# Performance work log

Hardware: AMD Instinct MI355X
Metric: run time of the kernel (lower is better)

## Reference

```python
import jax, jax.numpy as jnp
import numpy as np

NUM_HEADS = 16

def setup_inputs() -> dict:
    B, S, H = 2, 2048, 1024
    Hh = H // 2
    key = jax.random.key(0)
    ks = jax.random.split(key, 16)
    sd = 1.0 / np.sqrt(H)
    sdh = 1.0 / np.sqrt(Hh)
    return {
        "query": jax.random.normal(ks[0], (B, S, H), jnp.float32),
        "key_in": jax.random.normal(ks[1], (B, S, H), jnp.float32),
        "value": jax.random.normal(ks[2], (B, S, H), jnp.float32),
        "direction_signal": jax.random.randint(ks[3], (B, S), 0, 3, jnp.int64),
        # Linear weights stored as (in, out); y = x @ W + b (same math as torch x @ W.T + b)
        "Wq_w": jax.random.normal(ks[4], (H, H), jnp.float32) * sd,
        "Wq_b": jnp.zeros((H,), jnp.float32),
        "Wk_w": jax.random.normal(ks[5], (H, H), jnp.float32) * sd,
        "Wk_b": jnp.zeros((H,), jnp.float32),
        "Wv_w": jax.random.normal(ks[6], (H, H), jnp.float32) * sd,
        "Wv_b": jnp.zeros((H,), jnp.float32),
        "ds1_w": jax.random.normal(ks[7], (H, Hh), jnp.float32) * sd,
        "ds1_b": jnp.zeros((Hh,), jnp.float32),
        "ds2_w": jax.random.normal(ks[8], (Hh, NUM_HEADS), jnp.float32) * sdh,
        "ds2_b": jnp.zeros((NUM_HEADS,), jnp.float32),
        "fo_w": jax.random.normal(ks[9], (H, H), jnp.float32) * sd,
        "fo_b": jnp.zeros((H,), jnp.float32),
    }

def reference(query, key_in, value, direction_signal,
              Wq_w, Wq_b, Wk_w, Wk_b, Wv_w, Wv_b,
              ds1_w, ds1_b, ds2_w, ds2_b, fo_w, fo_b):
    B, S, H = query.shape
    nh = NUM_HEADS
    hd = H // nh
    scale = np.sqrt(hd).astype(np.float32)

    def split_heads(x):  # (B,S,H) -> (B,nh,S,hd)
        return x.reshape(B, S, nh, hd).transpose(0, 2, 1, 3)

    Q = split_heads(query @ Wq_w + Wq_b)
    K = split_heads(key_in @ Wk_w + Wk_b)
    V = split_heads(value @ Wv_w + Wv_b)

    scores = jnp.einsum('bhqd,bhkd->bhqk', Q, K) / scale

    # direction bias: per-(batch, head, query) additive scalar broadcast over keys
    # torch nn.GELU default is exact (erf) -> approximate=False
    dir_w = jax.nn.gelu(query @ ds1_w + ds1_b, approximate=False) @ ds2_w + ds2_b  # (B,S,nh)
    scores = scores + 0.3 * dir_w.transpose(0, 2, 1)[..., None]

    attention = jax.nn.softmax(scores, axis=-1)
    # dropout is identity in eval/reference mode
    context = jnp.einsum('bhqk,bhkd->bqhd', attention, V).reshape(B, S, H)
    output = context @ fo_w + fo_b
    return output, attention
```

## Files before the change

### kernel.cpp

```cpp
#include <hip/hip_runtime.h>


typedef unsigned short u16;
typedef unsigned int   u32;
typedef _Float16       f16;
typedef f16   half8   __attribute__((ext_vector_type(8)));
typedef float floatx4 __attribute__((ext_vector_type(4)));
typedef u32   u32x4   __attribute__((ext_vector_type(4)));

union V8 { u16 u[8]; u32x4 v; };

__device__ __forceinline__ u16 f16_bits(float f){
    union { f16 h; u16 u; } x; x.h = (f16)f; return x.u;
}

template<typename TI>
__global__ __launch_bounds__(256) void transpose_k(
    const TI* __restrict__ in, u16* __restrict__ out,
    long irs, long ors, int zdiv, long ibs0, long ibs1, long obs0, long obs1)
{
    __shared__ u16 tile[64][72];
    int z = blockIdx.z;
    const TI* ip = in  + (long)(z / zdiv) * ibs0 + (long)(z % zdiv) * ibs1;
    u16*      op = out + (long)(z / zdiv) * obs0 + (long)(z % zdiv) * obs1;
    long r0 = (long)blockIdx.y * 64, c0 = (long)blockIdx.x * 64;
    int t = threadIdx.x;
    int r = t >> 2, cs = (t & 3) * 16;
#pragma unroll
    for (int j = 0; j < 16; j++){
        TI v = ip[(r0 + r) * irs + c0 + cs + j];
        if (sizeof(TI) == 4) tile[r][cs + j] = f16_bits((float)v);
        else                 tile[r][cs + j] = (u16)v;
    }
    __syncthreads();
#pragma unroll
    for (int j = 0; j < 16; j++){
        op[(c0 + r) * ors + r0 + cs + j] = tile[cs + j][r];
    }
}

__global__ __launch_bounds__(256) void transpose_w4(
    const float* __restrict__ w0, const float* __restrict__ w1,
    const float* __restrict__ w2, const float* __restrict__ w3,
    u16* __restrict__ o0, u16* __restrict__ o1,
    u16* __restrict__ o2, u16* __restrict__ o3)
{
    __shared__ u16 tile[64][72];
    int z = blockIdx.z;
    const float* ip = (z == 0) ? w0 : (z == 1) ? w1 : (z == 2) ? w2 : w3;
    u16*         op = (z == 0) ? o0 : (z == 1) ? o1 : (z == 2) ? o2 : o3;
    long r0 = (long)blockIdx.y * 64, c0 = (long)blockIdx.x * 64;
    int t = threadIdx.x;
    int r = t >> 2, cs = (t & 3) * 16;
#pragma unroll
    for (int j = 0; j < 16; j++)
        tile[r][cs + j] = f16_bits(ip[(r0 + r) * 1024 + c0 + cs + j]);
    __syncthreads();
#pragma unroll
    for (int j = 0; j < 16; j++)
        op[(c0 + r) * 1024 + r0 + cs + j] = tile[cs + j][r];
}

template<bool A_F32, bool OUT_F32>
__global__ __launch_bounds__(256) void gemm_bt(
    const void* __restrict__ Av, const u16* __restrict__ BT,
    const float* __restrict__ bias, void* __restrict__ Cv,
    int M, int N, int K, float out_scale)
{
    __shared__ u16 Alds[64][40];
    __shared__ u16 Blds[64][40];
    int m0 = blockIdx.y * 64, n0 = blockIdx.x * 64;
    int t = threadIdx.x, w = t >> 6, lane = t & 63, quad = lane >> 4, l16 = lane & 15;
    int wm = (w >> 1) * 32, wn = (w & 1) * 32;
    const floatx4 zero4 = {0.f, 0.f, 0.f, 0.f};
    floatx4 acc[2][2];
#pragma unroll
    for (int i = 0; i < 2; i++)
#pragma unroll
        for (int j = 0; j < 2; j++) acc[i][j] = zero4;

    int srow = t >> 2, scol = (t & 3) * 8;
    const float* Apf = (const float*)Av + (long)(m0 + srow) * K + scol;
    const u16*   Aph = (const u16*)Av   + (long)(m0 + srow) * K + scol;
    const u16*   Bp  = BT + (long)(n0 + srow) * K + scol;

    for (int k0 = 0; k0 < K; k0 += 32){
        __syncthreads();
        V8 va, vb;
        if (A_F32){
            floatx4 a0 = *(const floatx4*)(Apf + k0);
            floatx4 a1 = *(const floatx4*)(Apf + k0 + 4);
#pragma unroll
            for (int j = 0; j < 4; j++){
                va.u[j]     = f16_bits(a0[j]);
                va.u[4 + j] = f16_bits(a1[j]);
            }
        } else {
            va.v = *(const u32x4*)(Aph + k0);
        }
        vb.v = *(const u32x4*)(Bp + k0);
        *(u32x4*)&Alds[srow][scol] = va.v;
        *(u32x4*)&Blds[srow][scol] = vb.v;
        __syncthreads();
        half8 a0 = *(const half8*)&Alds[wm + l16][quad * 8];
        half8 a1 = *(const half8*)&Alds[wm + 16 + l16][quad * 8];
        half8 b0 = *(const half8*)&Blds[wn + l16][quad * 8];
        half8 b1 = *(const half8*)&Blds[wn + 16 + l16][quad * 8];
        acc[0][0] = __builtin_amdgcn_mfma_f32_16x16x32_f16(a0, b0, acc[0][0], 0, 0, 0);
        acc[0][1] = __builtin_amdgcn_mfma_f32_16x16x32_f16(a0, b1, acc[0][1], 0, 0, 0);
        acc[1][0] = __builtin_amdgcn_mfma_f32_16x16x32_f16(a1, b0, acc[1][0], 0, 0, 0);
        acc[1][1] = __builtin_amdgcn_mfma_f32_16x16x32_f16(a1, b1, acc[1][1], 0, 0, 0);
    }

#pragma unroll
    for (int mi = 0; mi < 2; mi++)
#pragma unroll
        for (int ni = 0; ni < 2; ni++){
            int n = n0 + wn + ni * 16 + l16;
            float bv = bias[n];
#pragma unroll
            for (int r = 0; r < 4; r++){
                int m = m0 + wm + mi * 16 + quad * 4 + r;
                float v = (acc[mi][ni][r] + bv) * out_scale;
                if (OUT_F32) ((float*)Cv)[(long)m * N + n] = v;
                else         ((u16*)Cv)[(long)m * N + n]   = f16_bits(v);
            }
        }
}

__global__ __launch_bounds__(256) void gemm_qkv(
    const float* __restrict__ Aq, const float* __restrict__ Ak, const float* __restrict__ Avv,
    const u16* __restrict__ Bq, const u16* __restrict__ Bk, const u16* __restrict__ Bv,
    const float* __restrict__ bq, const float* __restrict__ bk, const float* __restrict__ bv,
    u16* __restrict__ Cq, u16* __restrict__ Ck, u16* __restrict__ Cv,
    int M, int N, int K)
{
    __shared__ u16 Alds[64][40];
    __shared__ u16 Blds[64][40];
    int z = blockIdx.z;
    const float* A    = (z == 0) ? Aq : (z == 1) ? Ak : Avv;
    const u16*   BT   = (z == 0) ? Bq : (z == 1) ? Bk : Bv;
    const float* bias = (z == 0) ? bq : (z == 1) ? bk : bv;
    u16*         C    = (z == 0) ? Cq : (z == 1) ? Ck : Cv;
    float out_scale   = (z == 0) ? 0.125f : 1.0f;

    int m0 = blockIdx.y * 64, n0 = blockIdx.x * 64;
    int t = threadIdx.x, w = t >> 6, lane = t & 63, quad = lane >> 4, l16 = lane & 15;
    int wm = (w >> 1) * 32, wn = (w & 1) * 32;
    const floatx4 zero4 = {0.f, 0.f, 0.f, 0.f};
    floatx4 acc[2][2];
#pragma unroll
    for (int i = 0; i < 2; i++)
#pragma unroll
        for (int j = 0; j < 2; j++) acc[i][j] = zero4;

    int srow = t >> 2, scol = (t & 3) * 8;
    const float* Apf = A + (long)(m0 + srow) * K + scol;
    const u16*   Bp  = BT + (long)(n0 + srow) * K + scol;

    for (int k0 = 0; k0 < K; k0 += 32){
        __syncthreads();
        V8 va, vb;
        floatx4 a0 = *(const floatx4*)(Apf + k0);
        floatx4 a1 = *(const floatx4*)(Apf + k0 + 4);
#pragma unroll
        for (int j = 0; j < 4; j++){
            va.u[j]     = f16_bits(a0[j]);
            va.u[4 + j] = f16_bits(a1[j]);
        }
        vb.v = *(const u32x4*)(Bp + k0);
        *(u32x4*)&Alds[srow][scol] = va.v;
        *(u32x4*)&Blds[srow][scol] = vb.v;
        __syncthreads();
        half8 af0 = *(const half8*)&Alds[wm + l16][quad * 8];
        half8 af1 = *(const half8*)&Alds[wm + 16 + l16][quad * 8];
        half8 bf0 = *(const half8*)&Blds[wn + l16][quad * 8];
        half8 bf1 = *(const half8*)&Blds[wn + 16 + l16][quad * 8];
        acc[0][0] = __builtin_amdgcn_mfma_f32_16x16x32_f16(af0, bf0, acc[0][0], 0, 0, 0);
        acc[0][1] = __builtin_amdgcn_mfma_f32_16x16x32_f16(af0, bf1, acc[0][1], 0, 0, 0);
        acc[1][0] = __builtin_amdgcn_mfma_f32_16x16x32_f16(af1, bf0, acc[1][0], 0, 0, 0);
        acc[1][1] = __builtin_amdgcn_mfma_f32_16x16x32_f16(af1, bf1, acc[1][1], 0, 0, 0);
    }

#pragma unroll
    for (int mi = 0; mi < 2; mi++)
#pragma unroll
        for (int ni = 0; ni < 2; ni++){
            int n = n0 + wn + ni * 16 + l16;
            float bv = bias[n];
#pragma unroll
            for (int r = 0; r < 4; r++){
                int m = m0 + wm + mi * 16 + quad * 4 + r;
                C[(long)m * N + n] = f16_bits((acc[mi][ni][r] + bv) * out_scale);
            }
        }
}

#define S_LEN 2048
#define NH 16
#define HD 64

__global__ __launch_bounds__(256) void attn_k(
    const u16* __restrict__ Q, const u16* __restrict__ K,
    const u16* __restrict__ VT, float* __restrict__ attn,
    u16* __restrict__ ctx)
{
    __shared__ u16 Klds[64][72];
    __shared__ u16 Vlds[64][72];
    __shared__ u16 P0  [64][72];
    __shared__ u16 P1  [64][72];

    int bx0 = blockIdx.x;
    int bx = ((bx0 & 7) << 6) | (bx0 >> 3);
    int qb = bx & 15, h = (bx >> 4) & 15, b = bx >> 8;
    int qbase = qb * 128;
    int t = threadIdx.x, w = t >> 6, lane = t & 63, quad = lane >> 4, l16 = lane & 15;
    const u16* Qp  = Q + (long)b * S_LEN * 1024 + h * HD;
    const u16* Kp  = K + (long)b * S_LEN * 1024 + h * HD;
    const u16* VTp = VT + ((long)(b * NH + h)) * HD * S_LEN;

    const u16* q0p = Qp + (long)(qbase + w * 16 + l16) * 1024;
    const u16* q1p = q0p + 64 * 1024;
    half8 qa0 = *(const half8*)(q0p + quad * 8);
    half8 qa1 = *(const half8*)(q0p + 32 + quad * 8);
    half8 qb0 = *(const half8*)(q1p + quad * 8);
    half8 qb1 = *(const half8*)(q1p + 32 + quad * 8);

    const floatx4 zero4 = {0.f, 0.f, 0.f, 0.f};
    int srow = t >> 2, sseg = (t & 3) * 16;

    const u16* kptr = Kp + (long)srow * 1024 + sseg;
    const u16* vptr = VTp + (long)srow * S_LEN + sseg;

    float lsum0 = 0.f, lsum1 = 0.f;
    {
        u32x4 pk0 = *(const u32x4*)(kptr);
        u32x4 pk1 = *(const u32x4*)(kptr + 8);
        const u16* kp = kptr + 64 * 1024;
        for (int it = 0; it < 32; ++it){
            __syncthreads();
            *(u32x4*)&Klds[srow][sseg]     = pk0;
            *(u32x4*)&Klds[srow][sseg + 8] = pk1;
            __syncthreads();
            if (it < 31){
                pk0 = *(const u32x4*)(kp);
                pk1 = *(const u32x4*)(kp + 8);
                kp += 64 * 1024;
            }
#pragma unroll
            for (int kt = 0; kt < 4; kt++){
                half8 kf0 = *(const half8*)&Klds[kt * 16 + l16][quad * 8];
                half8 kf1 = *(const half8*)&Klds[kt * 16 + l16][32 + quad * 8];
                floatx4 s0 = __builtin_amdgcn_mfma_f32_16x16x32_f16(kf0, qa0, zero4, 0, 0, 0);
                s0 = __builtin_amdgcn_mfma_f32_16x16x32_f16(kf1, qa1, s0, 0, 0, 0);
                floatx4 s1 = __builtin_amdgcn_mfma_f32_16x16x32_f16(kf0, qb0, zero4, 0, 0, 0);
                s1 = __builtin_amdgcn_mfma_f32_16x16x32_f16(kf1, qb1, s1, 0, 0, 0);
#pragma unroll
                for (int r = 0; r < 4; r++){
                    lsum0 += __expf(s0[r]);
                    lsum1 += __expf(s1[r]);
                }
            }
        }
    }
    lsum0 += __shfl_xor(lsum0, 16); lsum0 += __shfl_xor(lsum0, 32);
    lsum1 += __shfl_xor(lsum1, 16); lsum1 += __shfl_xor(lsum1, 32);
    float linv0 = 1.f / lsum0, linv1 = 1.f / lsum1;

    floatx4 cta[4], ctb[4];
#pragma unroll
    for (int dt = 0; dt < 4; dt++){ cta[dt] = zero4; ctb[dt] = zero4; }

    long aq0 = ((long)(b * NH + h) * S_LEN + qbase + w * 16 + l16) * S_LEN;
    long aq1 = aq0 + 64L * S_LEN;

    {
        u32x4 pk0 = *(const u32x4*)(kptr);
        u32x4 pk1 = *(const u32x4*)(kptr + 8);
        u32x4 pv0 = *(const u32x4*)(vptr);
        u32x4 pv1 = *(const u32x4*)(vptr + 8);
        const u16* kp = kptr + 64 * 1024;
        const u16* vp = vptr + 64;
        for (int it = 0; it < 32; ++it){
            int k0 = it * 64;
            __syncthreads();
            *(u32x4*)&Klds[srow][sseg]     = pk0;
            *(u32x4*)&Klds[srow][sseg + 8] = pk1;
            *(u32x4*)&Vlds[srow][sseg]     = pv0;
            *(u32x4*)&Vlds[srow][sseg + 8] = pv1;
            __syncthreads();
            if (it < 31){
                pk0 = *(const u32x4*)(kp);
                pk1 = *(const u32x4*)(kp + 8);
                pv0 = *(const u32x4*)(vp);
                pv1 = *(const u32x4*)(vp + 8);
                kp += 64 * 1024;
                vp += 64;
            }
#pragma unroll
            for (int kt = 0; kt < 4; kt++){
                half8 kf0 = *(const half8*)&Klds[kt * 16 + l16][quad * 8];
                half8 kf1 = *(const half8*)&Klds[kt * 16 + l16][32 + quad * 8];
                floatx4 s0 = __builtin_amdgcn_mfma_f32_16x16x32_f16(kf0, qa0, zero4, 0, 0, 0);
                s0 = __builtin_amdgcn_mfma_f32_16x16x32_f16(kf1, qa1, s0, 0, 0, 0);
                floatx4 s1 = __builtin_amdgcn_mfma_f32_16x16x32_f16(kf0, qb0, zero4, 0, 0, 0);
                s1 = __builtin_amdgcn_mfma_f32_16x16x32_f16(kf1, qb1, s1, 0, 0, 0);
                floatx4 p0;
#pragma unroll
                for (int r = 0; r < 4; r++) p0[r] = __expf(s0[r]) * linv0;
                __builtin_nontemporal_store(p0,
                    (floatx4*)(attn + aq0 + k0 + kt * 16 + quad * 4));
                u32 pa01 = (u32)f16_bits(p0[0]) | ((u32)f16_bits(p0[1]) << 16);
                u32 pa23 = (u32)f16_bits(p0[2]) | ((u32)f16_bits(p0[3]) << 16);
                *(u32*)&P0[w * 16 + l16][kt * 16 + quad * 4]     = pa01;
                *(u32*)&P0[w * 16 + l16][kt * 16 + quad * 4 + 2] = pa23;
                floatx4 p1;
#pragma unroll
                for (int r = 0; r < 4; r++) p1[r] = __expf(s1[r]) * linv1;
                __builtin_nontemporal_store(p1,
                    (floatx4*)(attn + aq1 + k0 + kt * 16 + quad * 4));
                u32 pb01 = (u32)f16_bits(p1[0]) | ((u32)f16_bits(p1[1]) << 16);
                u32 pb23 = (u32)f16_bits(p1[2]) | ((u32)f16_bits(p1[3]) << 16);
                *(u32*)&P1[w * 16 + l16][kt * 16 + quad * 4]     = pb01;
                *(u32*)&P1[w * 16 + l16][kt * 16 + quad * 4 + 2] = pb23;
            }
#pragma unroll
            for (int kk = 0; kk < 2; kk++){
                half8 pf0 = *(const half8*)&P0[w * 16 + l16][kk * 32 + quad * 8];
                half8 pf1 = *(const half8*)&P1[w * 16 + l16][kk * 32 + quad * 8];
#pragma unroll
                for (int dt = 0; dt < 4; dt++){
                    half8 vf = *(const half8*)&Vlds[dt * 16 + l16][kk * 32 + quad * 8];
                    cta[dt] = __builtin_amdgcn_mfma_f32_16x16x32_f16(vf, pf0, cta[dt], 0, 0, 0);
                    ctb[dt] = __builtin_amdgcn_mfma_f32_16x16x32_f16(vf, pf1, ctb[dt], 0, 0, 0);
                }
            }
        }
    }

#pragma unroll
    for (int dt = 0; dt < 4; dt++)
#pragma unroll
        for (int r = 0; r < 4; r++){
            P0[w * 16 + l16][dt * 16 + quad * 4 + r] = f16_bits(cta[dt][r]);
            P1[w * 16 + l16][dt * 16 + quad * 4 + r] = f16_bits(ctb[dt][r]);
        }
    __syncthreads();
    {
        V8 o0, o1, o2, o3;
#pragma unroll
        for (int j = 0; j < 8; j++){
            o0.u[j] = P0[srow][sseg + j];
            o1.u[j] = P0[srow][sseg + 8 + j];
            o2.u[j] = P1[srow][sseg + j];
            o3.u[j] = P1[srow][sseg + 8 + j];
        }
        long c0 = ((long)b * S_LEN + qbase + srow) * 1024 + h * HD + sseg;
        long c1 = c0 + 64L * 1024;
        *(u32x4*)(ctx + c0)     = o0.v;
        *(u32x4*)(ctx + c0 + 8) = o1.v;
        *(u32x4*)(ctx + c1)     = o2.v;
        *(u32x4*)(ctx + c1 + 8) = o3.v;
    }
}

extern "C" void kernel_launch(void* const* d_in, const int* in_sizes, int n_in,
                              void* d_out, int out_size, void* d_ws, size_t ws_size,
                              hipStream_t stream)
{
    (void)in_sizes; (void)n_in; (void)out_size; (void)ws_size;
    const float* query  = (const float*)d_in[0];
    const float* key_in = (const float*)d_in[1];
    const float* value  = (const float*)d_in[2];
    const float* Wq_w = (const float*)d_in[4];  const float* Wq_b = (const float*)d_in[5];
    const float* Wk_w = (const float*)d_in[6];  const float* Wk_b = (const float*)d_in[7];
    const float* Wv_w = (const float*)d_in[8];  const float* Wv_b = (const float*)d_in[9];
    const float* fo_w = (const float*)d_in[14]; const float* fo_b = (const float*)d_in[15];

    float* out  = (float*)d_out;
    float* attn = out + 4194304L;

    u16* ws  = (u16*)d_ws;
    u16* WqT = ws;
    u16* WkT = WqT + 1048576;
    u16* WvT = WkT + 1048576;
    u16* foT = WvT + 1048576;
    u16* Qm  = foT + 1048576;
    u16* Km  = Qm  + 4194304;
    u16* Vm  = Km  + 4194304;
    u16* VTm = Vm  + 4194304;
    u16* CTX = VTm + 4194304;

    dim3 blk(256);
    transpose_w4<<<dim3(16,16,4), blk, 0, stream>>>(
        Wq_w, Wk_w, Wv_w, fo_w, WqT, WkT, WvT, foT);
    gemm_qkv<<<dim3(16,64,3), blk, 0, stream>>>(
        query, key_in, value, WqT, WkT, WvT, Wq_b, Wk_b, Wv_b,
        Qm, Km, Vm, 4096, 1024, 1024);
    transpose_k<u16><<<dim3(1,32,32), blk, 0, stream>>>(Vm, VTm, 1024, 2048, 16,
        2048L*1024, 64, 16L*64*2048, 64L*2048);
    attn_k<<<dim3(512), blk, 0, stream>>>(Qm, Km, VTm, attn, CTX);
    gemm_bt<false,true><<<dim3(16,64), blk, 0, stream>>>(CTX, foT, fo_b, out, 4096,1024,1024, 1.0f);
}
```

Measured before the change: 818.5 us.

## Use 128x128 GEMM tiles with direct global-to-LDS loads and exp2 softmax

The QKV and output projection GEMMs move from 64x64 to 128x128 block tiles with 4x4 MFMA accumulators per wave, and half-precision operands are loaded straight into LDS with global_load_lds. The attention kernel switches from __expf to the hardware exp2, with log2(e) folded into the Q projection scale, and packs probabilities to fp16 with cvt_pkrtz. The aim is more data reuse per LDS load, fewer conversion instructions, and cheaper exponentials. In exchange, LDS is unpadded (possible bank conflicts), there is more register pressure, and the GEMM grids are smaller.

After: 794.9 us. -2.9%, faster.

```diff
diff --git a/kernel.cpp b/kernel.cpp
--- a/kernel.cpp
+++ b/kernel.cpp
@@ -5,14 +5,21 @@
 typedef unsigned int   u32;
 typedef _Float16       f16;
 typedef f16   half8   __attribute__((ext_vector_type(8)));
+typedef f16   h2f16   __attribute__((ext_vector_type(2)));
 typedef float floatx4 __attribute__((ext_vector_type(4)));
 typedef u32   u32x4   __attribute__((ext_vector_type(4)));
+typedef u32   u32x2   __attribute__((ext_vector_type(2)));
 
 union V8 { u16 u[8]; u32x4 v; };
 
 __device__ __forceinline__ u16 f16_bits(float f){
     union { f16 h; u16 u; } x; x.h = (f16)f; return x.u;
 }
+
+#define GLDS16(gsrc, ldst) \
+    __builtin_amdgcn_global_load_lds( \
+        (const __attribute__((address_space(1))) void*)(gsrc), \
+        (__attribute__((address_space(3))) void*)(ldst), 16, 0, 0)
 
 template<typename TI>
 __global__ __launch_bounds__(256) void transpose_k(
@@ -62,138 +69,116 @@
 }
 
 template<bool A_F32, bool OUT_F32>
-__global__ __launch_bounds__(256) void gemm_bt(
+__device__ __forceinline__ void gemm128_body(
     const void* __restrict__ Av, const u16* __restrict__ BT,
     const float* __restrict__ bias, void* __restrict__ Cv,
-    int M, int N, int K, float out_scale)
-{
-    __shared__ u16 Alds[64][40];
-    __shared__ u16 Blds[64][40];
-    int m0 = blockIdx.y * 64, n0 = blockIdx.x * 64;
+    int M, int N, int K, float out_scale,
+    u16* Ald, u16* Bld, int m0, int n0)
+{
     int t = threadIdx.x, w = t >> 6, lane = t & 63, quad = lane >> 4, l16 = lane & 15;
-    int wm = (w >> 1) * 32, wn = (w & 1) * 32;
+    int wm = (w >> 1) * 64, wn = (w & 1) * 64;
     const floatx4 zero4 = {0.f, 0.f, 0.f, 0.f};
-    floatx4 acc[2][2];
-#pragma unroll
-    for (int i = 0; i < 2; i++)
-#pragma unroll
-        for (int j = 0; j < 2; j++) acc[i][j] = zero4;
-
-    int srow = t >> 2, scol = (t & 3) * 8;
-    const float* Apf = (const float*)Av + (long)(m0 + srow) * K + scol;
-    const u16*   Aph = (const u16*)Av   + (long)(m0 + srow) * K + scol;
-    const u16*   Bp  = BT + (long)(n0 + srow) * K + scol;
+    floatx4 acc[4][4];
+#pragma unroll
+    for (int i = 0; i < 4; i++)
+#pragma unroll
+        for (int j = 0; j < 4; j++) acc[i][j] = zero4;
+
+    int grow = w * 16 + (lane >> 2);
+    int gcol = (lane & 3) * 8;
+    const u16* Bsrc0 = BT + (long)(n0 + grow) * K + gcol;
+    const u16* Bsrc1 = BT + (long)(n0 + 64 + grow) * K + gcol;
+    u16* Bdst0 = Bld + w * 512;
+    u16* Bdst1 = Bld + 2048 + w * 512;
+
+    int arow = t >> 1, acol = (t & 1) * 16;
+    const float* Afp = (const float*)Av + (long)(m0 + arow) * K + acol;
+    u16* Adst = Ald + arow * 32 + acol;
+    const u16* Asrc0 = (const u16*)Av + (long)(m0 + grow) * K + gcol;
+    const u16* Asrc1 = (const u16*)Av + (long)(m0 + 64 + grow) * K + gcol;
+    u16* Adst0 = Ald + w * 512;
+    u16* Adst1 = Ald + 2048 + w * 512;
 
     for (int k0 = 0; k0 < K; k0 += 32){
         __syncthreads();
-        V8 va, vb;
+        GLDS16(Bsrc0 + k0, Bdst0);
+        GLDS16(Bsrc1 + k0, Bdst1);
         if (A_F32){
-            floatx4 a0 = *(const floatx4*)(Apf + k0);
-            floatx4 a1 = *(const floatx4*)(Apf + k0 + 4);
+            floatx4 a0 = *(const floatx4*)(Afp + k0);
+            floatx4 a1 = *(const floatx4*)(Afp + k0 + 4);
+            floatx4 a2 = *(const floatx4*)(Afp + k0 + 8);
+            floatx4 a3 = *(const floatx4*)(Afp + k0 + 12);
+            V8 x, y;
 #pragma unroll
             for (int j = 0; j < 4; j++){
-                va.u[j]     = f16_bits(a0[j]);
-                va.u[4 + j] = f16_bits(a1[j]);
-            }
+                x.u[j] = f16_bits(a0[j]); x.u[4 + j] = f16_bits(a1[j]);
+                y.u[j] = f16_bits(a2[j]); y.u[4 + j] = f16_bits(a3[j]);
+            }
+            *(u32x4*)Adst       = x.v;
+            *(u32x4*)(Adst + 8) = y.v;
         } else {
-            va.v = *(const u32x4*)(Aph + k0);
-        }
-        vb.v = *(const u32x4*)(Bp + k0);
-        *(u32x4*)&Alds[srow][scol] = va.v;
-        *(u32x4*)&Blds[srow][scol] = vb.v;
+            GLDS16(Asrc0 + k0, Adst0);
+            GLDS16(Asrc1 + k0, Adst1);
+        }
         __syncthreads();
-        half8 a0 = *(const half8*)&Alds[wm + l16][quad * 8];
-        half8 a1 = *(const half8*)&Alds[wm + 16 + l16][quad * 8];
-        half8 b0 = *(const half8*)&Blds[wn + l16][quad * 8];
-        half8 b1 = *(const half8*)&Blds[wn + 16 + l16][quad * 8];
-        acc[0][0] = __builtin_amdgcn_mfma_f32_16x16x32_f16(a0, b0, acc[0][0], 0, 0, 0);
-        acc[0][1] = __builtin_amdgcn_mfma_f32_16x16x32_f16(a0, b1, acc[0][1], 0, 0, 0);
-        acc[1][0] = __builtin_amdgcn_mfma_f32_16x16x32_f16(a1, b0, acc[1][0], 0, 0, 0);
-        acc[1][1] = __builtin_amdgcn_mfma_f32_16x16x32_f16(a1, b1, acc[1][1], 0, 0, 0);
-    }
-
-#pragma unroll
-    for (int mi = 0; mi < 2; mi++)
-#pragma unroll
-        for (int ni = 0; ni < 2; ni++){
-            int n = n0 + wn + ni * 16 + l16;
+        half8 af[4], bf[4];
+#pragma unroll
+        for (int i = 0; i < 4; i++)
+            af[i] = *(const half8*)&Ald[(wm + i * 16 + l16) * 32 + quad * 8];
+#pragma unroll
+        for (int j = 0; j < 4; j++)
+            bf[j] = *(const half8*)&Bld[(wn + j * 16 + l16) * 32 + quad * 8];
+#pragma unroll
+        for (int i = 0; i < 4; i++)
+#pragma unroll
+            for (int j = 0; j < 4; j++)
+                acc[i][j] = __builtin_amdgcn_mfma_f32_16x16x32_f16(af[i], bf[j], acc[i][j], 0, 0, 0);
+    }
+
+#pragma unroll
+    for (int i = 0; i < 4; i++)
+#pragma unroll
+        for (int j = 0; j < 4; j++){
+            int n = n0 + wn + j * 16 + l16;
             float bv = bias[n];
 #pragma unroll
             for (int r = 0; r < 4; r++){
-                int m = m0 + wm + mi * 16 + quad * 4 + r;
-                float v = (acc[mi][ni][r] + bv) * out_scale;
+                int m = m0 + wm + i * 16 + quad * 4 + r;
+                float v = (acc[i][j][r] + bv) * out_scale;
                 if (OUT_F32) ((float*)Cv)[(long)m * N + n] = v;
                 else         ((u16*)Cv)[(long)m * N + n]   = f16_bits(v);
             }
         }
 }
 
-__global__ __launch_bounds__(256) void gemm_qkv(
+__global__ __launch_bounds__(256) void gemm128_qkv(
     const float* __restrict__ Aq, const float* __restrict__ Ak, const float* __restrict__ Avv,
     const u16* __restrict__ Bq, const u16* __restrict__ Bk, const u16* __restrict__ Bv,
     const float* __restrict__ bq, const float* __restrict__ bk, const float* __restrict__ bv,
     u16* __restrict__ Cq, u16* __restrict__ Ck, u16* __restrict__ Cv,
     int M, int N, int K)
 {
-    __shared__ u16 Alds[64][40];
-    __shared__ u16 Blds[64][40];
+    __shared__ u16 Ald[4096];
+    __shared__ u16 Bld[4096];
     int z = blockIdx.z;
     const float* A    = (z == 0) ? Aq : (z == 1) ? Ak : Avv;
     const u16*   BT   = (z == 0) ? Bq : (z == 1) ? Bk : Bv;
     const float* bias = (z == 0) ? bq : (z == 1) ? bk : bv;
     u16*         C    = (z == 0) ? Cq : (z == 1) ? Ck : Cv;
-    float out_scale   = (z == 0) ? 0.125f : 1.0f;
-
-    int m0 = blockIdx.y * 64, n0 = blockIdx.x * 64;
-    int t = threadIdx.x, w = t >> 6, lane = t & 63, quad = lane >> 4, l16 = lane & 15;
-    int wm = (w >> 1) * 32, wn = (w & 1) * 32;
-    const floatx4 zero4 = {0.f, 0.f, 0.f, 0.f};
-    floatx4 acc[2][2];
-#pragma unroll
-    for (int i = 0; i < 2; i++)
-#pragma unroll
-        for (int j = 0; j < 2; j++) acc[i][j] = zero4;
-
-    int srow = t >> 2, scol = (t & 3) * 8;
-    const float* Apf = A + (long)(m0 + srow) * K + scol;
-    const u16*   Bp  = BT + (long)(n0 + srow) * K + scol;
-
-    for (int k0 = 0; k0 < K; k0 += 32){
-        __syncthreads();
-        V8 va, vb;
-        floatx4 a0 = *(const floatx4*)(Apf + k0);
-        floatx4 a1 = *(const floatx4*)(Apf + k0 + 4);
-#pragma unroll
-        for (int j = 0; j < 4; j++){
-            va.u[j]     = f16_bits(a0[j]);
-            va.u[4 + j] = f16_bits(a1[j]);
-        }
-        vb.v = *(const u32x4*)(Bp + k0);
-        *(u32x4*)&Alds[srow][scol] = va.v;
-        *(u32x4*)&Blds[srow][scol] = vb.v;
-        __syncthreads();
-        half8 af0 = *(const half8*)&Alds[wm + l16][quad * 8];
-        half8 af1 = *(const half8*)&Alds[wm + 16 + l16][quad * 8];
-        half8 bf0 = *(const half8*)&Blds[wn + l16][quad * 8];
-        half8 bf1 = *(const half8*)&Blds[wn + 16 + l16][quad * 8];
-        acc[0][0] = __builtin_amdgcn_mfma_f32_16x16x32_f16(af0, bf0, acc[0][0], 0, 0, 0);
-        acc[0][1] = __builtin_amdgcn_mfma_f32_16x16x32_f16(af0, bf1, acc[0][1], 0, 0, 0);
-        acc[1][0] = __builtin_amdgcn_mfma_f32_16x16x32_f16(af1, bf0, acc[1][0], 0, 0, 0);
-        acc[1][1] = __builtin_amdgcn_mfma_f32_16x16x32_f16(af1, bf1, acc[1][1], 0, 0, 0);
-    }
-
-#pragma unroll
-    for (int mi = 0; mi < 2; mi++)
-#pragma unroll
-        for (int ni = 0; ni < 2; ni++){
-            int n = n0 + wn + ni * 16 + l16;
-            float bv = bias[n];
-#pragma unroll
-            for (int r = 0; r < 4; r++){
-                int m = m0 + wm + mi * 16 + quad * 4 + r;
-                C[(long)m * N + n] = f16_bits((acc[mi][ni][r] + bv) * out_scale);
-            }
-        }
+    float scale       = (z == 0) ? 0.125f * 1.4426950408889634f : 1.0f;
+    gemm128_body<true, false>(A, BT, bias, C, M, N, K, scale,
+                              Ald, Bld, blockIdx.y * 128, blockIdx.x * 128);
+}
+
+__global__ __launch_bounds__(256) void gemm128_ctx(
+    const u16* __restrict__ A, const u16* __restrict__ BT,
+    const float* __restrict__ bias, float* __restrict__ C,
+    int M, int N, int K)
+{
+    __shared__ u16 Ald[4096];
+    __shared__ u16 Bld[4096];
+    gemm128_body<false, true>(A, BT, bias, C, M, N, K, 1.0f,
+                              Ald, Bld, blockIdx.y * 128, blockIdx.x * 128);
 }
 
 #define S_LEN 2048
@@ -257,8 +242,8 @@
                 s1 = __builtin_amdgcn_mfma_f32_16x16x32_f16(kf1, qb1, s1, 0, 0, 0);
 #pragma unroll
                 for (int r = 0; r < 4; r++){
-                    lsum0 += __expf(s0[r]);
-                    lsum1 += __expf(s1[r]);
+                    lsum0 += __builtin_amdgcn_exp2f(s0[r]);
+                    lsum1 += __builtin_amdgcn_exp2f(s1[r]);
                 }
             }
         }
@@ -307,22 +292,22 @@
                 s1 = __builtin_amdgcn_mfma_f32_16x16x32_f16(kf1, qb1, s1, 0, 0, 0);
                 floatx4 p0;
 #pragma unroll
-                for (int r = 0; r < 4; r++) p0[r] = __expf(s0[r]) * linv0;
+                for (int r = 0; r < 4; r++) p0[r] = __builtin_amdgcn_exp2f(s0[r]) * linv0;
                 __builtin_nontemporal_store(p0,
                     (floatx4*)(attn + aq0 + k0 + kt * 16 + quad * 4));
-                u32 pa01 = (u32)f16_bits(p0[0]) | ((u32)f16_bits(p0[1]) << 16);
-                u32 pa23 = (u32)f16_bits(p0[2]) | ((u32)f16_bits(p0[3]) << 16);
-                *(u32*)&P0[w * 16 + l16][kt * 16 + quad * 4]     = pa01;
-                *(u32*)&P0[w * 16 + l16][kt * 16 + quad * 4 + 2] = pa23;
+                u32x2 pw0;
+                pw0[0] = __builtin_bit_cast(u32, __builtin_amdgcn_cvt_pkrtz(p0[0], p0[1]));
+                pw0[1] = __builtin_bit_cast(u32, __builtin_amdgcn_cvt_pkrtz(p0[2], p0[3]));
+                *(u32x2*)&P0[w * 16 + l16][kt * 16 + quad * 4] = pw0;
                 floatx4 p1;
 #pragma unroll
-                for (int r = 0; r < 4; r++) p1[r] = __expf(s1[r]) * linv1;
+                for (int r = 0; r < 4; r++) p1[r] = __builtin_amdgcn_exp2f(s1[r]) * linv1;
                 __builtin_nontemporal_store(p1,
                     (floatx4*)(attn + aq1 + k0 + kt * 16 + quad * 4));
-                u32 pb01 = (u32)f16_bits(p1[0]) | ((u32)f16_bits(p1[1]) << 16);
-                u32 pb23 = (u32)f16_bits(p1[2]) | ((u32)f16_bits(p1[3]) << 16);
-                *(u32*)&P1[w * 16 + l16][kt * 16 + quad * 4]     = pb01;
-                *(u32*)&P1[w * 16 + l16][kt * 16 + quad * 4 + 2] = pb23;
+                u32x2 pw1;
+                pw1[0] = __builtin_bit_cast(u32, __builtin_amdgcn_cvt_pkrtz(p1[0], p1[1]));
+                pw1[1] = __builtin_bit_cast(u32, __builtin_amdgcn_cvt_pkrtz(p1[2], p1[3]));
+                *(u32x2*)&P1[w * 16 + l16][kt * 16 + quad * 4] = pw1;
             }
 #pragma unroll
             for (int kk = 0; kk < 2; kk++){
@@ -394,11 +379,11 @@
     dim3 blk(256);
     transpose_w4<<<dim3(16,16,4), blk, 0, stream>>>(
         Wq_w, Wk_w, Wv_w, fo_w, WqT, WkT, WvT, foT);
-    gemm_qkv<<<dim3(16,64,3), blk, 0, stream>>>(
+    gemm128_qkv<<<dim3(8,32,3), blk, 0, stream>>>(
         query, key_in, value, WqT, WkT, WvT, Wq_b, Wk_b, Wv_b,
         Qm, Km, Vm, 4096, 1024, 1024);
     transpose_k<u16><<<dim3(1,32,32), blk, 0, stream>>>(Vm, VTm, 1024, 2048, 16,
         2048L*1024, 64, 16L*64*2048, 64L*2048);
     attn_k<<<dim3(512), blk, 0, stream>>>(Qm, Km, VTm, attn, CTX);
-    gemm_bt<false,true><<<dim3(16,64), blk, 0, stream>>>(CTX, foT, fo_b, out, 4096,1024,1024, 1.0f);
-}
+    gemm128_ctx<<<dim3(8,32), blk, 0, stream>>>(CTX, foT, fo_b, out, 4096, 1024, 1024);
+}
```
